# Optimization experiments

Measured on AMD Instinct MI355X. Metric: run time of the kernel, lower is better.

Reference implementation:

```python
import jax, jax.numpy as jnp
import numpy as np

B, S, D, H = 2, 2048, 1024, 16
DK = D // H


def setup_inputs() -> dict:
    key = jax.random.key(0)
    ks = jax.random.split(key, 12)
    scale = 0.02
    inp = {
        "query": jax.random.normal(ks[0], (B, S, D), jnp.float32),
        "key": jax.random.normal(ks[1], (B, S, D), jnp.float32),
        "value": jax.random.normal(ks[2], (B, S, D), jnp.float32),
        "mask": jax.random.randint(ks[3], (B, S), 0, 2, jnp.int32),
        "Wq": jax.random.normal(ks[4], (D, D), jnp.float32) * scale,
        "bq": jnp.zeros((D,), jnp.float32),
        "Wk": jax.random.normal(ks[5], (D, D), jnp.float32) * scale,
        "bk": jnp.zeros((D,), jnp.float32),
        "Wv": jax.random.normal(ks[6], (D, D), jnp.float32) * scale,
        "bv": jnp.zeros((D,), jnp.float32),
        "Wo": jax.random.normal(ks[7], (D, D), jnp.float32) * scale,
        "bo": jnp.zeros((D,), jnp.float32),
    }
    return inp


def reference(query, key, value, mask, Wq, bq, Wk, bk, Wv, bv, Wo, bo):
    # Linear projections then split heads: [B, S, D] -> [B, H, S, DK]
    def proj(x, W, b):
        y = x @ W.T + b  # torch nn.Linear: x @ W^T + b
        return y.reshape(B, S, H, DK).transpose(0, 2, 1, 3)

    q = proj(query, Wq, bq)
    k = proj(key, Wk, bk)
    v = proj(value, Wv, bv)

    # Scaled dot-product attention with full [B, H, S, S] scores (naive form)
    scores = jnp.einsum("bhqd,bhkd->bhqk", q, k) / jnp.sqrt(jnp.float32(DK))
    # mask==1 marks padding over key positions; broadcast [B,1,1,S]
    pad = (mask == 1)[:, None, None, :]
    scores = jnp.where(pad, -jnp.inf, scores)
    p_attn = jax.nn.softmax(scores, axis=-1)
    # dropout omitted (eval / deterministic mode)
    x = jnp.einsum("bhqk,bhkd->bhqd", p_attn, v)
    x = x.transpose(0, 2, 1, 3).reshape(B, S, D)
    return x @ Wo.T + bo
```

## Files before the change

kernel.cpp:

```cpp
#include <hip/hip_runtime.h>
#include <stdint.h>

typedef short bf16x8 __attribute__((ext_vector_type(8)));
typedef float f32x4  __attribute__((ext_vector_type(4)));
typedef unsigned short u16;

#define BB 2
#define SS 2048
#define DD 1024
#define HH 16
#define NTOK (BB*SS)

__device__ __forceinline__ u16 f2bf(float f) {
  union { float f; uint32_t u; } c; c.f = f;
  uint32_t r = c.u + 0x7FFFu + ((c.u >> 16) & 1u);
  return (u16)(r >> 16);
}

__device__ __forceinline__ void gll16(const void* g, void* l) {
  __builtin_amdgcn_global_load_lds((__attribute__((address_space(1))) void*)(void*)g,
                                   (__attribute__((address_space(3))) void*)l, 16, 0, 0);
}

__global__ void cvt_kernel(const float* __restrict__ src, u16* __restrict__ dst, int n) {
  int i = (blockIdx.x * blockDim.x + threadIdx.x) * 4;
  const int stride = gridDim.x * blockDim.x * 4;
  for (; i < n; i += stride) {
    float4 v = *(const float4*)(src + i);
    ushort4 o;
    o.x = f2bf(v.x); o.y = f2bf(v.y); o.z = f2bf(v.z); o.w = f2bf(v.w);
    *(ushort4*)(dst + i) = o;
  }
}

template<bool OUT_F32>
__device__ __forceinline__ void gemm_bt_body(const u16* __restrict__ A,
                                             const u16* __restrict__ W,
                                             const float* __restrict__ bias,
                                             void* __restrict__ Cout) {
  __shared__ __align__(16) u16 As[128 * 32];
  __shared__ __align__(16) u16 Bs[128 * 32];
  const int tid = threadIdx.x;
  const int lane = tid & 63, wid = tid >> 6;
  const int r16 = lane & 15, g4 = lane >> 4;
  const int m0 = blockIdx.y * 128, n0 = blockIdx.x * 128;
  const int wm = (wid >> 1) * 64, wn = (wid & 1) * 64;

  const f32x4 zero = {0.f, 0.f, 0.f, 0.f};
  f32x4 acc[4][4];
#pragma unroll
  for (int i = 0; i < 4; ++i)
#pragma unroll
    for (int j = 0; j < 4; ++j) acc[i][j] = zero;

  const int row0 = tid >> 2, blk0 = tid & 3;
  for (int k0 = 0; k0 < DD; k0 += 32) {
#pragma unroll
    for (int it = 0; it < 2; ++it) {
      const int row = row0 + it * 64;
      const int sb = blk0 ^ (row & 3);
      gll16(A + (size_t)(m0 + row) * DD + k0 + sb * 8, As + (tid + it * 256) * 8);
      gll16(W + (size_t)(n0 + row) * DD + k0 + sb * 8, Bs + (tid + it * 256) * 8);
    }
    __syncthreads();
    bf16x8 af[4], bfr[4];
#pragma unroll
    for (int i = 0; i < 4; ++i) {
      const int ar = wm + i * 16 + r16;
      af[i] = *(const bf16x8*)(As + ar * 32 + ((g4 ^ (ar & 3)) << 3));
      const int br = wn + i * 16 + r16;
      bfr[i] = *(const bf16x8*)(Bs + br * 32 + ((g4 ^ (br & 3)) << 3));
    }
#pragma unroll
    for (int i = 0; i < 4; ++i)
#pragma unroll
      for (int j = 0; j < 4; ++j)
        acc[i][j] = __builtin_amdgcn_mfma_f32_16x16x32_bf16(af[i], bfr[j], acc[i][j], 0, 0, 0);
    __syncthreads();
  }
#pragma unroll
  for (int j = 0; j < 4; ++j) {
    const int col = n0 + wn + j * 16 + r16;
    const float bj = bias[col];
#pragma unroll
    for (int i = 0; i < 4; ++i) {
      const int rowb = m0 + wm + i * 16 + g4 * 4;
#pragma unroll
      for (int r = 0; r < 4; ++r) {
        const float v = acc[i][j][r] + bj;
        if (OUT_F32)
          ((float*)Cout)[(size_t)(rowb + r) * DD + col] = v;
        else
          ((u16*)Cout)[(size_t)(rowb + r) * DD + col] = f2bf(v);
      }
    }
  }
}

struct QkvArgs {
  const u16* A[3];
  const u16* W[3];
  const float* bias[3];
  u16* out[3];
};

__global__ __launch_bounds__(256) void gemm_qkv_kernel(QkvArgs args) {
  const int z = blockIdx.z;
  gemm_bt_body<false>(args.A[z], args.W[z], args.bias[z], (void*)args.out[z]);
}

__global__ __launch_bounds__(256) void gemm_out_kernel(const u16* __restrict__ A,
                                                       const u16* __restrict__ W,
                                                       const float* __restrict__ bias,
                                                       float* __restrict__ C) {
  gemm_bt_body<true>(A, W, bias, (void*)C);
}

__global__ __launch_bounds__(256) void transpose_kernel(const u16* __restrict__ in,
                                                        u16* __restrict__ out) {
  __shared__ u16 tile[64][68];
  const int s0 = blockIdx.x * 64, d0 = blockIdx.y * 64, b = blockIdx.z;
  const int t = threadIdx.x;
#pragma unroll
  for (int it = 0; it < 2; ++it) {
    const int tt = t + it * 256;
    const int sl = tt >> 3, dc = (tt & 7) << 3;
    bf16x8 v = *(const bf16x8*)(in + (size_t)(b * SS + s0 + sl) * DD + d0 + dc);
#pragma unroll
    for (int i = 0; i < 8; ++i) tile[sl][dc + i] = v[i];
  }
  __syncthreads();
#pragma unroll
  for (int it = 0; it < 2; ++it) {
    const int tt = t + it * 256;
    const int dl = tt >> 3, sc = (tt & 7) << 3;
    bf16x8 v;
#pragma unroll
    for (int i = 0; i < 8; ++i) v[i] = tile[sc + i][dl];
    *(bf16x8*)(out + (size_t)(b * DD + d0 + dl) * SS + s0 + sc) = v;
  }
}

#define LOG2E_SCALE 0.18033688f
#define PSTR 88
__global__ __launch_bounds__(256) void attn_kernel(const u16* __restrict__ Qp,
                                                   const u16* __restrict__ Kp,
                                                   const u16* __restrict__ Vt,
                                                   const int* __restrict__ mask,
                                                   u16* __restrict__ ctx) {
  __shared__ __align__(16) u16 Ks[64 * 64];
  __shared__ __align__(16) u16 Vs[64 * 64];
  __shared__ __align__(16) u16 Ps[4][16 * PSTR];
  __shared__ float maskadd[64];

  const int tid = threadIdx.x;
  const int lane = tid & 63, wid = tid >> 6;
  const int r16 = lane & 15, g4 = lane >> 4;
  const int qt = blockIdx.x, h = blockIdx.y, b = blockIdx.z;

  const int qtok = b * SS + qt * 64 + wid * 16 + r16;
  bf16x8 qf[2];
#pragma unroll
  for (int c = 0; c < 2; ++c)
    qf[c] = *(const bf16x8*)(Qp + (size_t)qtok * DD + h * 64 + c * 32 + g4 * 8);

  const f32x4 zero = {0.f, 0.f, 0.f, 0.f};
  f32x4 o[4];
#pragma unroll
  for (int j = 0; j < 4; ++j) o[j] = zero;
  float lrow[4];
#pragma unroll
  for (int r = 0; r < 4; ++r) lrow[r] = 0.f;

  const int srow0 = tid >> 3, sblk0 = tid & 7;
  for (int kt = 0; kt < SS / 64; ++kt) {
#pragma unroll
    for (int it = 0; it < 2; ++it) {
      const int row = srow0 + it * 32;
      const int sb = sblk0 ^ (row & 7);
      gll16(Kp + (size_t)(b * SS + kt * 64 + row) * DD + h * 64 + sb * 8,
            Ks + (tid + it * 256) * 8);
      gll16(Vt + (size_t)(b * DD + h * 64 + row) * SS + kt * 64 + sb * 8,
            Vs + (tid + it * 256) * 8);
    }
    if (tid < 64) {
      const int mv = mask[b * SS + kt * 64 + tid];
      maskadd[tid] = (mv == 1) ? -1e30f : 0.f;
    }
    __syncthreads();

    f32x4 s[4];
#pragma unroll
    for (int j = 0; j < 4; ++j) s[j] = zero;
#pragma unroll
    for (int c = 0; c < 2; ++c)
#pragma unroll
      for (int j = 0; j < 4; ++j) {
        const int kr = j * 16 + r16;
        const bf16x8 kf = *(const bf16x8*)(Ks + kr * 64 + (((c * 4 + g4) ^ (kr & 7)) << 3));
        s[j] = __builtin_amdgcn_mfma_f32_16x16x32_bf16(qf[c], kf, s[j], 0, 0, 0);
      }

    float p[4][4];
#pragma unroll
    for (int j = 0; j < 4; ++j) {
      const float ma = maskadd[j * 16 + r16];
#pragma unroll
      for (int r = 0; r < 4; ++r) p[j][r] = exp2f(fmaf(s[j][r], LOG2E_SCALE, ma));
    }
#pragma unroll
    for (int r = 0; r < 4; ++r)
      lrow[r] += (p[0][r] + p[1][r]) + (p[2][r] + p[3][r]);

    u16* pw = &Ps[wid][0];
#pragma unroll
    for (int j = 0; j < 4; ++j)
#pragma unroll
      for (int r = 0; r < 4; r += 2) {
        uint32_t pk;
        asm("v_cvt_pk_bf16_f32 %0, %1, %2" : "=v"(pk) : "v"(p[j][r]), "v"(p[j][r + 1]));
        pw[(g4 * 4 + r) * PSTR + j * 16 + r16] = (u16)pk;
        pw[(g4 * 4 + r + 1) * PSTR + j * 16 + r16] = (u16)(pk >> 16);
      }
    asm volatile("s_waitcnt lgkmcnt(0)" ::: "memory");
    __builtin_amdgcn_sched_barrier(0);

    bf16x8 pa[2];
#pragma unroll
    for (int c = 0; c < 2; ++c)
      pa[c] = *(const bf16x8*)(pw + r16 * PSTR + c * 32 + g4 * 8);
#pragma unroll
    for (int c = 0; c < 2; ++c)
#pragma unroll
      for (int j = 0; j < 4; ++j) {
        const int vr = j * 16 + r16;
        const bf16x8 vf = *(const bf16x8*)(Vs + vr * 64 + (((c * 4 + g4) ^ (vr & 7)) << 3));
        o[j] = __builtin_amdgcn_mfma_f32_16x16x32_bf16(pa[c], vf, o[j], 0, 0, 0);
      }
    __syncthreads();
  }

#pragma unroll
  for (int r = 0; r < 4; ++r) {
#pragma unroll
    for (int off = 8; off; off >>= 1) lrow[r] += __shfl_xor(lrow[r], off);
  }

  const int otok = b * SS + qt * 64 + wid * 16 + g4 * 4;
  float inv[4];
#pragma unroll
  for (int r = 0; r < 4; ++r) inv[r] = 1.0f / lrow[r];
#pragma unroll
  for (int j = 0; j < 4; ++j) {
    const int col = h * 64 + j * 16 + r16;
#pragma unroll
    for (int r = 0; r < 4; ++r) {
      const float v = o[j][r] * inv[r];
      ctx[(size_t)(otok + r) * DD + col] = f2bf(v);
    }
  }
}

extern "C" void kernel_launch(void* const* d_in, const int* in_sizes, int n_in,
                              void* d_out, int out_size, void* d_ws, size_t ws_size,
                              hipStream_t stream) {
  (void)in_sizes; (void)n_in; (void)out_size; (void)ws_size;
  const float* f_q = (const float*)d_in[0];
  const float* f_k = (const float*)d_in[1];
  const float* f_v = (const float*)d_in[2];
  const int* mask  = (const int*)d_in[3];
  const float* Wq = (const float*)d_in[4];
  const float* bq = (const float*)d_in[5];
  const float* Wk = (const float*)d_in[6];
  const float* bk = (const float*)d_in[7];
  const float* Wv = (const float*)d_in[8];
  const float* bv = (const float*)d_in[9];
  const float* Wo = (const float*)d_in[10];
  const float* bo = (const float*)d_in[11];

  char* ws = (char*)d_ws;
  const size_t XB = (size_t)NTOK * DD * 2;
  const size_t WB = (size_t)DD * DD * 2;
  u16* Xq  = (u16*)(ws);
  u16* Xk  = (u16*)(ws + XB);
  u16* Xv  = (u16*)(ws + 2 * XB);
  u16* Qp  = (u16*)(ws + 3 * XB);
  u16* Kp  = (u16*)(ws + 4 * XB);
  u16* Vp  = (u16*)(ws + 5 * XB);
  u16* Wqb = (u16*)(ws + 6 * XB);
  u16* Wkb = (u16*)(ws + 6 * XB + WB);
  u16* Wvb = (u16*)(ws + 6 * XB + 2 * WB);
  u16* Wob = (u16*)(ws + 6 * XB + 3 * WB);
  u16* Vt  = Xq;
  u16* ctx = Xk;

  cvt_kernel<<<2048, 256, 0, stream>>>(f_q, Xq, NTOK * DD);
  cvt_kernel<<<2048, 256, 0, stream>>>(f_k, Xk, NTOK * DD);
  cvt_kernel<<<2048, 256, 0, stream>>>(f_v, Xv, NTOK * DD);
  cvt_kernel<<<1024, 256, 0, stream>>>(Wq, Wqb, DD * DD);
  cvt_kernel<<<1024, 256, 0, stream>>>(Wk, Wkb, DD * DD);
  cvt_kernel<<<1024, 256, 0, stream>>>(Wv, Wvb, DD * DD);
  cvt_kernel<<<1024, 256, 0, stream>>>(Wo, Wob, DD * DD);

  QkvArgs qa;
  qa.A[0] = Xq;  qa.A[1] = Xk;  qa.A[2] = Xv;
  qa.W[0] = Wqb; qa.W[1] = Wkb; qa.W[2] = Wvb;
  qa.bias[0] = bq; qa.bias[1] = bk; qa.bias[2] = bv;
  qa.out[0] = Qp; qa.out[1] = Kp; qa.out[2] = Vp;
  gemm_qkv_kernel<<<dim3(DD / 128, NTOK / 128, 3), 256, 0, stream>>>(qa);

  transpose_kernel<<<dim3(SS / 64, DD / 64, BB), 256, 0, stream>>>(Vp, Vt);
  attn_kernel<<<dim3(SS / 64, HH, BB), 256, 0, stream>>>(Qp, Kp, Vt, mask, ctx);
  gemm_out_kernel<<<dim3(DD / 128, NTOK / 128), 256, 0, stream>>>(ctx, Wob, bo, (float*)d_out);
}
```

Baseline: 171.1 us.

## Fold mask and scaling into QKV epilogue, drop transpose, double-buffer attention

The Q projection epilogue now premultiplies by the softmax scale times log2e. The K and V epilogues zero masked token rows, and V is written directly in transposed layout, which removes the separate transpose kernel and the per-tile mask handling in attention. Because masked keys now contribute exp(0)=1 to the row sum, a small kernel counts padded tokens so attention can subtract that count from the denominator. Attention also double-buffers the K and V tiles to overlap loads with MFMA work, swaps MFMA operand order so each lane holds a full row sum, and uses a swizzled packed-dword P buffer. The seven conversion launches are merged into two batched launches. The risk is reduced precision in the denominator subtraction when most keys are padded, and extra shared memory from the second buffer.

```diff
diff --git a/kernel.cpp b/kernel.cpp
--- a/kernel.cpp
+++ b/kernel.cpp
@@ -10,6 +10,7 @@
 #define DD 1024
 #define HH 16
 #define NTOK (BB*SS)
+#define QSC 0.18033688f
 
 __device__ __forceinline__ u16 f2bf(float f) {
   union { float f; uint32_t u; } c; c.f = f;
@@ -22,10 +23,13 @@
                                    (__attribute__((address_space(3))) void*)l, 16, 0, 0);
 }
 
-__global__ void cvt_kernel(const float* __restrict__ src, u16* __restrict__ dst, int n) {
+struct CvtArgs { const float* src[4]; u16* dst[4]; int n; };
+__global__ void cvtn_kernel(CvtArgs a) {
+  const float* __restrict__ src = a.src[blockIdx.z];
+  u16* __restrict__ dst = a.dst[blockIdx.z];
   int i = (blockIdx.x * blockDim.x + threadIdx.x) * 4;
   const int stride = gridDim.x * blockDim.x * 4;
-  for (; i < n; i += stride) {
+  for (; i < a.n; i += stride) {
     float4 v = *(const float4*)(src + i);
     ushort4 o;
     o.x = f2bf(v.x); o.y = f2bf(v.y); o.z = f2bf(v.z); o.w = f2bf(v.w);
@@ -33,10 +37,25 @@
   }
 }
 
-template<bool OUT_F32>
+__global__ __launch_bounds__(256) void maskcnt_kernel(const int* __restrict__ mask,
+                                                      float* __restrict__ out) {
+  const int b = blockIdx.x, t = threadIdx.x;
+  const int4 v1 = *(const int4*)(mask + b * SS + t * 8);
+  const int4 v2 = *(const int4*)(mask + b * SS + t * 8 + 4);
+  int s = v1.x + v1.y + v1.z + v1.w + v2.x + v2.y + v2.z + v2.w;
+#pragma unroll
+  for (int off = 32; off; off >>= 1) s += __shfl_xor(s, off);
+  __shared__ int red[4];
+  if ((t & 63) == 0) red[t >> 6] = s;
+  __syncthreads();
+  if (t == 0) out[b] = (float)(red[0] + red[1] + red[2] + red[3]);
+}
+
+template<int MODE>
 __device__ __forceinline__ void gemm_bt_body(const u16* __restrict__ A,
                                              const u16* __restrict__ W,
                                              const float* __restrict__ bias,
+                                             const int* __restrict__ mask,
                                              void* __restrict__ Cout) {
   __shared__ __align__(16) u16 As[128 * 32];
   __shared__ __align__(16) u16 Bs[128 * 32];
@@ -78,20 +97,44 @@
         acc[i][j] = __builtin_amdgcn_mfma_f32_16x16x32_bf16(af[i], bfr[j], acc[i][j], 0, 0, 0);
     __syncthreads();
   }
-#pragma unroll
-  for (int j = 0; j < 4; ++j) {
-    const int col = n0 + wn + j * 16 + r16;
-    const float bj = bias[col];
-#pragma unroll
-    for (int i = 0; i < 4; ++i) {
-      const int rowb = m0 + wm + i * 16 + g4 * 4;
-#pragma unroll
-      for (int r = 0; r < 4; ++r) {
-        const float v = acc[i][j][r] + bj;
-        if (OUT_F32)
-          ((float*)Cout)[(size_t)(rowb + r) * DD + col] = v;
-        else
+
+  float bcol[4];
+#pragma unroll
+  for (int j = 0; j < 4; ++j) bcol[j] = bias[n0 + wn + j * 16 + r16];
+
+#pragma unroll
+  for (int i = 0; i < 4; ++i) {
+    const int rowb = m0 + wm + i * 16 + g4 * 4;
+    int mr[4] = {0, 0, 0, 0};
+    if (MODE == 1 || MODE == 2) {
+      const int4 mv = *(const int4*)(mask + rowb);
+      mr[0] = mv.x; mr[1] = mv.y; mr[2] = mv.z; mr[3] = mv.w;
+    }
+#pragma unroll
+    for (int j = 0; j < 4; ++j) {
+      const int col = n0 + wn + j * 16 + r16;
+      if (MODE == 3) {
+#pragma unroll
+        for (int r = 0; r < 4; ++r)
+          ((float*)Cout)[(size_t)(rowb + r) * DD + col] = acc[i][j][r] + bcol[j];
+      } else if (MODE == 0) {
+#pragma unroll
+        for (int r = 0; r < 4; ++r)
+          ((u16*)Cout)[(size_t)(rowb + r) * DD + col] = f2bf((acc[i][j][r] + bcol[j]) * QSC);
+      } else if (MODE == 1) {
+#pragma unroll
+        for (int r = 0; r < 4; ++r) {
+          const float v = mr[r] ? 0.f : (acc[i][j][r] + bcol[j]);
           ((u16*)Cout)[(size_t)(rowb + r) * DD + col] = f2bf(v);
+        }
+      } else {
+        const int bb = rowb >> 11, s0 = rowb & (SS - 1);
+        ushort4 pk;
+        pk.x = f2bf(mr[0] ? 0.f : (acc[i][j][0] + bcol[j]));
+        pk.y = f2bf(mr[1] ? 0.f : (acc[i][j][1] + bcol[j]));
+        pk.z = f2bf(mr[2] ? 0.f : (acc[i][j][2] + bcol[j]));
+        pk.w = f2bf(mr[3] ? 0.f : (acc[i][j][3] + bcol[j]));
+        *(ushort4*)((u16*)Cout + (size_t)(bb * DD + col) * SS + s0) = pk;
       }
     }
   }
@@ -101,57 +144,32 @@
   const u16* A[3];
   const u16* W[3];
   const float* bias[3];
-  u16* out[3];
+  const int* mask;
+  u16* outq; u16* outk; u16* outv;
 };
 
-__global__ __launch_bounds__(256) void gemm_qkv_kernel(QkvArgs args) {
+__global__ __launch_bounds__(256) void gemm_qkv_kernel(QkvArgs a) {
   const int z = blockIdx.z;
-  gemm_bt_body<false>(args.A[z], args.W[z], args.bias[z], (void*)args.out[z]);
+  if (z == 0)      gemm_bt_body<0>(a.A[0], a.W[0], a.bias[0], nullptr, (void*)a.outq);
+  else if (z == 1) gemm_bt_body<1>(a.A[1], a.W[1], a.bias[1], a.mask, (void*)a.outk);
+  else             gemm_bt_body<2>(a.A[2], a.W[2], a.bias[2], a.mask, (void*)a.outv);
 }
 
 __global__ __launch_bounds__(256) void gemm_out_kernel(const u16* __restrict__ A,
                                                        const u16* __restrict__ W,
                                                        const float* __restrict__ bias,
                                                        float* __restrict__ C) {
-  gemm_bt_body<true>(A, W, bias, (void*)C);
-}
-
-__global__ __launch_bounds__(256) void transpose_kernel(const u16* __restrict__ in,
-                                                        u16* __restrict__ out) {
-  __shared__ u16 tile[64][68];
-  const int s0 = blockIdx.x * 64, d0 = blockIdx.y * 64, b = blockIdx.z;
-  const int t = threadIdx.x;
-#pragma unroll
-  for (int it = 0; it < 2; ++it) {
-    const int tt = t + it * 256;
-    const int sl = tt >> 3, dc = (tt & 7) << 3;
-    bf16x8 v = *(const bf16x8*)(in + (size_t)(b * SS + s0 + sl) * DD + d0 + dc);
-#pragma unroll
-    for (int i = 0; i < 8; ++i) tile[sl][dc + i] = v[i];
-  }
-  __syncthreads();
-#pragma unroll
-  for (int it = 0; it < 2; ++it) {
-    const int tt = t + it * 256;
-    const int dl = tt >> 3, sc = (tt & 7) << 3;
-    bf16x8 v;
-#pragma unroll
-    for (int i = 0; i < 8; ++i) v[i] = tile[sc + i][dl];
-    *(bf16x8*)(out + (size_t)(b * DD + d0 + dl) * SS + s0 + sc) = v;
-  }
-}
-
-#define LOG2E_SCALE 0.18033688f
-#define PSTR 88
+  gemm_bt_body<3>(A, W, bias, nullptr, (void*)C);
+}
+
 __global__ __launch_bounds__(256) void attn_kernel(const u16* __restrict__ Qp,
                                                    const u16* __restrict__ Kp,
                                                    const u16* __restrict__ Vt,
-                                                   const int* __restrict__ mask,
+                                                   const float* __restrict__ padcnt,
                                                    u16* __restrict__ ctx) {
-  __shared__ __align__(16) u16 Ks[64 * 64];
-  __shared__ __align__(16) u16 Vs[64 * 64];
-  __shared__ __align__(16) u16 Ps[4][16 * PSTR];
-  __shared__ float maskadd[64];
+  __shared__ __align__(16) u16 Ks[2][64 * 64];
+  __shared__ __align__(16) u16 Vs[2][64 * 64];
+  __shared__ __align__(16) uint32_t Ps[4][16 * 32];
 
   const int tid = threadIdx.x;
   const int lane = tid & 63, wid = tid >> 6;
@@ -168,96 +186,95 @@
   f32x4 o[4];
 #pragma unroll
   for (int j = 0; j < 4; ++j) o[j] = zero;
-  float lrow[4];
-#pragma unroll
-  for (int r = 0; r < 4; ++r) lrow[r] = 0.f;
+  float ll = 0.f;
 
   const int srow0 = tid >> 3, sblk0 = tid & 7;
-  for (int kt = 0; kt < SS / 64; ++kt) {
+  const u16* Kbase = Kp + (size_t)(b * SS) * DD + h * 64;
+  const u16* Vbase = Vt + (size_t)(b * DD + h * 64) * SS;
+
+  auto stage = [&](int kt, int buf) {
 #pragma unroll
     for (int it = 0; it < 2; ++it) {
       const int row = srow0 + it * 32;
       const int sb = sblk0 ^ (row & 7);
-      gll16(Kp + (size_t)(b * SS + kt * 64 + row) * DD + h * 64 + sb * 8,
-            Ks + (tid + it * 256) * 8);
-      gll16(Vt + (size_t)(b * DD + h * 64 + row) * SS + kt * 64 + sb * 8,
-            Vs + (tid + it * 256) * 8);
-    }
-    if (tid < 64) {
-      const int mv = mask[b * SS + kt * 64 + tid];
-      maskadd[tid] = (mv == 1) ? -1e30f : 0.f;
-    }
-    __syncthreads();
-
-    f32x4 s[4];
-#pragma unroll
-    for (int j = 0; j < 4; ++j) s[j] = zero;
+      gll16(Kbase + (size_t)(kt * 64 + row) * DD + sb * 8, &Ks[buf][(tid + it * 256) * 8]);
+      gll16(Vbase + (size_t)row * SS + kt * 64 + sb * 8, &Vs[buf][(tid + it * 256) * 8]);
+    }
+  };
+
+  stage(0, 0);
+  __syncthreads();
+
+  for (int kt = 0; kt < SS / 64; ++kt) {
+    const int cur = kt & 1;
+    if (kt + 1 < SS / 64) stage(kt + 1, cur ^ 1);
+
+    f32x4 st[4];
+#pragma unroll
+    for (int j = 0; j < 4; ++j) st[j] = zero;
 #pragma unroll
     for (int c = 0; c < 2; ++c)
 #pragma unroll
       for (int j = 0; j < 4; ++j) {
         const int kr = j * 16 + r16;
-        const bf16x8 kf = *(const bf16x8*)(Ks + kr * 64 + (((c * 4 + g4) ^ (kr & 7)) << 3));
-        s[j] = __builtin_amdgcn_mfma_f32_16x16x32_bf16(qf[c], kf, s[j], 0, 0, 0);
+        const bf16x8 kf = *(const bf16x8*)(&Ks[cur][kr * 64 + (((c * 4 + g4) ^ (kr & 7)) << 3)]);
+        st[j] = __builtin_amdgcn_mfma_f32_16x16x32_bf16(kf, qf[c], st[j], 0, 0, 0);
       }
 
-    float p[4][4];
+    uint32_t pk[4][2];
 #pragma unroll
     for (int j = 0; j < 4; ++j) {
-      const float ma = maskadd[j * 16 + r16];
-#pragma unroll
-      for (int r = 0; r < 4; ++r) p[j][r] = exp2f(fmaf(s[j][r], LOG2E_SCALE, ma));
-    }
-#pragma unroll
-    for (int r = 0; r < 4; ++r)
-      lrow[r] += (p[0][r] + p[1][r]) + (p[2][r] + p[3][r]);
-
-    u16* pw = &Ps[wid][0];
-#pragma unroll
-    for (int j = 0; j < 4; ++j)
-#pragma unroll
-      for (int r = 0; r < 4; r += 2) {
-        uint32_t pk;
-        asm("v_cvt_pk_bf16_f32 %0, %1, %2" : "=v"(pk) : "v"(p[j][r]), "v"(p[j][r + 1]));
-        pw[(g4 * 4 + r) * PSTR + j * 16 + r16] = (u16)pk;
-        pw[(g4 * 4 + r + 1) * PSTR + j * 16 + r16] = (u16)(pk >> 16);
-      }
+      float p0, p1, p2, p3;
+      asm("v_exp_f32 %0, %1" : "=v"(p0) : "v"(st[j][0]));
+      asm("v_exp_f32 %0, %1" : "=v"(p1) : "v"(st[j][1]));
+      asm("v_exp_f32 %0, %1" : "=v"(p2) : "v"(st[j][2]));
+      asm("v_exp_f32 %0, %1" : "=v"(p3) : "v"(st[j][3]));
+      ll += (p0 + p1) + (p2 + p3);
+      asm("v_cvt_pk_bf16_f32 %0, %1, %2" : "=v"(pk[j][0]) : "v"(p0), "v"(p1));
+      asm("v_cvt_pk_bf16_f32 %0, %1, %2" : "=v"(pk[j][1]) : "v"(p2), "v"(p3));
+    }
+
+    uint32_t* pw = &Ps[wid][0];
+    const int swz = (r16 & 7) << 2;
+#pragma unroll
+    for (int j = 0; j < 4; ++j) {
+      pw[r16 * 32 + ((j * 8 + g4 * 2) ^ swz)] = pk[j][0];
+      pw[r16 * 32 + ((j * 8 + g4 * 2 + 1) ^ swz)] = pk[j][1];
+    }
     asm volatile("s_waitcnt lgkmcnt(0)" ::: "memory");
     __builtin_amdgcn_sched_barrier(0);
 
     bf16x8 pa[2];
 #pragma unroll
     for (int c = 0; c < 2; ++c)
-      pa[c] = *(const bf16x8*)(pw + r16 * PSTR + c * 32 + g4 * 8);
+      pa[c] = *(const bf16x8*)(pw + r16 * 32 + (((c * 16 + g4 * 4)) ^ swz));
+
 #pragma unroll
     for (int c = 0; c < 2; ++c)
 #pragma unroll
       for (int j = 0; j < 4; ++j) {
         const int vr = j * 16 + r16;
-        const bf16x8 vf = *(const bf16x8*)(Vs + vr * 64 + (((c * 4 + g4) ^ (vr & 7)) << 3));
+        const bf16x8 vf = *(const bf16x8*)(&Vs[cur][vr * 64 + (((c * 4 + g4) ^ (vr & 7)) << 3)]);
         o[j] = __builtin_amdgcn_mfma_f32_16x16x32_bf16(pa[c], vf, o[j], 0, 0, 0);
       }
     __syncthreads();
   }
 
-#pragma unroll
-  for (int r = 0; r < 4; ++r) {
-#pragma unroll
-    for (int off = 8; off; off >>= 1) lrow[r] += __shfl_xor(lrow[r], off);
-  }
+  ll += __shfl_xor(ll, 16);
+  ll += __shfl_xor(ll, 32);
+  ll -= padcnt[b];
+  const float inv = 1.0f / ll;
+  float invr[4];
+#pragma unroll
+  for (int r = 0; r < 4; ++r) invr[r] = __shfl(inv, g4 * 4 + r);
 
   const int otok = b * SS + qt * 64 + wid * 16 + g4 * 4;
-  float inv[4];
-#pragma unroll
-  for (int r = 0; r < 4; ++r) inv[r] = 1.0f / lrow[r];
 #pragma unroll
   for (int j = 0; j < 4; ++j) {
     const int col = h * 64 + j * 16 + r16;
 #pragma unroll
-    for (int r = 0; r < 4; ++r) {
-      const float v = o[j][r] * inv[r];
-      ctx[(size_t)(otok + r) * DD + col] = f2bf(v);
-    }
+    for (int r = 0; r < 4; ++r)
+      ctx[(size_t)(otok + r) * DD + col] = f2bf(o[j][r] * invr[r]);
   }
 }
 
@@ -286,30 +303,36 @@
   u16* Xv  = (u16*)(ws + 2 * XB);
   u16* Qp  = (u16*)(ws + 3 * XB);
   u16* Kp  = (u16*)(ws + 4 * XB);
-  u16* Vp  = (u16*)(ws + 5 * XB);
+  u16* Vt  = (u16*)(ws + 5 * XB);
   u16* Wqb = (u16*)(ws + 6 * XB);
   u16* Wkb = (u16*)(ws + 6 * XB + WB);
   u16* Wvb = (u16*)(ws + 6 * XB + 2 * WB);
   u16* Wob = (u16*)(ws + 6 * XB + 3 * WB);
-  u16* Vt  = Xq;
-  u16* ctx = Xk;
-
-  cvt_kernel<<<2048, 256, 0, stream>>>(f_q, Xq, NTOK * DD);
-  cvt_kernel<<<2048, 256, 0, stream>>>(f_k, Xk, NTOK * DD);
-  cvt_kernel<<<2048, 256, 0, stream>>>(f_v, Xv, NTOK * DD);
-  cvt_kernel<<<1024, 256, 0, stream>>>(Wq, Wqb, DD * DD);
-  cvt_kernel<<<1024, 256, 0, stream>>>(Wk, Wkb, DD * DD);
-  cvt_kernel<<<1024, 256, 0, stream>>>(Wv, Wvb, DD * DD);
-  cvt_kernel<<<1024, 256, 0, stream>>>(Wo, Wob, DD * DD);
+  float* padcnt = (float*)(ws + 6 * XB + 4 * WB);
+  u16* ctx = Xq;
+
+  CvtArgs cx;
+  cx.src[0] = f_q; cx.src[1] = f_k; cx.src[2] = f_v; cx.src[3] = f_q;
+  cx.dst[0] = Xq;  cx.dst[1] = Xk;  cx.dst[2] = Xv;  cx.dst[3] = Xq;
+  cx.n = NTOK * DD;
+  cvtn_kernel<<<dim3(1024, 1, 3), 256, 0, stream>>>(cx);
+
+  CvtArgs cw;
+  cw.src[0] = Wq;  cw.src[1] = Wk;  cw.src[2] = Wv;  cw.src[3] = Wo;
+  cw.dst[0] = Wqb; cw.dst[1] = Wkb; cw.dst[2] = Wvb; cw.dst[3] = Wob;
+  cw.n = DD * DD;
+  cvtn_kernel<<<dim3(256, 1, 4), 256, 0, stream>>>(cw);
+
+  maskcnt_kernel<<<BB, 256, 0, stream>>>(mask, padcnt);
 
   QkvArgs qa;
   qa.A[0] = Xq;  qa.A[1] = Xk;  qa.A[2] = Xv;
   qa.W[0] = Wqb; qa.W[1] = Wkb; qa.W[2] = Wvb;
   qa.bias[0] = bq; qa.bias[1] = bk; qa.bias[2] = bv;
-  qa.out[0] = Qp; qa.out[1] = Kp; qa.out[2] = Vp;
+  qa.mask = mask;
+  qa.outq = Qp; qa.outk = Kp; qa.outv = Vt;
   gemm_qkv_kernel<<<dim3(DD / 128, NTOK / 128, 3), 256, 0, stream>>>(qa);
 
-  transpose_kernel<<<dim3(SS / 64, DD / 64, BB), 256, 0, stream>>>(Vp, Vt);
-  attn_kernel<<<dim3(SS / 64, HH, BB), 256, 0, stream>>>(Qp, Kp, Vt, mask, ctx);
+  attn_kernel<<<dim3(SS / 64, HH, BB), 256, 0, stream>>>(Qp, Kp, Vt, padcnt, ctx);
   gemm_out_kernel<<<dim3(DD / 128, NTOK / 128), 256, 0, stream>>>(ctx, Wob, bo, (float*)d_out);
 }
```

Measured after the change: 155.9 us. -8.9%, faster.
